# Kernel tuning notes

Hardware: AMD Instinct MI355X
Metric: run time of the kernel (lower is better)

## Reference

```python
import jax, jax.numpy as jnp
import numpy as np

B, Nq, Nk, R = 4, 1024, 1024, 256
NH, DK, DV = 8, 64, 64


def setup_inputs() -> dict:
    key = jax.random.key(0)
    ks = jax.random.split(key, 16)
    mk = lambda k, shape, s=1.0: jax.random.normal(k, shape, dtype=jnp.float32) * s
    inp = {
        'Q_real': mk(ks[0], (B, Nq, R)), 'Q_imag': mk(ks[1], (B, Nq, R)),
        'K_real': mk(ks[2], (B, Nk, R)), 'K_imag': mk(ks[3], (B, Nk, R)),
        'V_real': mk(ks[4], (B, Nk, R)), 'V_imag': mk(ks[5], (B, Nk, R)),
        'WQ_r': mk(ks[6], (NH * DK, R), 0.02), 'WQ_i': mk(ks[7], (NH * DK, R), 0.02),
        'WK_r': mk(ks[8], (NH * DK, R), 0.02), 'WK_i': mk(ks[9], (NH * DK, R), 0.02),
        'WV_r': mk(ks[10], (NH * DV, R), 0.02), 'WV_i': mk(ks[11], (NH * DV, R), 0.02),
        'WO_r': mk(ks[12], (R, NH * DV), 0.02), 'WO_i': mk(ks[13], (R, NH * DV), 0.02),
        'mask': jax.random.randint(ks[14], (B, Nk), 0, 2).astype(bool),
    }
    return inp


def _complex_linear(x, w_r, w_i):
    # x: complex [..., in]; weights real [out, in]. Same math as 4 real matmuls.
    w = (w_r + 1j * w_i).astype(jnp.complex64)
    return x @ w.T


def reference(Q_real, Q_imag, K_real, K_imag, V_real, V_imag,
              WQ_r, WQ_i, WK_r, WK_i, WV_r, WV_i, WO_r, WO_i, mask):
    Q = (Q_real + 1j * Q_imag).astype(jnp.complex64)
    K = (K_real + 1j * K_imag).astype(jnp.complex64)
    V = (V_real + 1j * V_imag).astype(jnp.complex64)

    Qp = _complex_linear(Q, WQ_r, WQ_i).reshape(B, Nq, NH, DK).transpose(0, 2, 1, 3)
    Kp = _complex_linear(K, WK_r, WK_i).reshape(B, Nk, NH, DK).transpose(0, 2, 1, 3)
    Vp = _complex_linear(V, WV_r, WV_i).reshape(B, Nk, NH, DV).transpose(0, 2, 1, 3)

    # complex scores [B, NH, Nq, Nk]; conj on K matches torch .conj().transpose
    scores = jnp.einsum('bhqd,bhkd->bhqk', Qp, jnp.conj(Kp)) / jnp.sqrt(jnp.float32(DK))
    scores_abs = jnp.abs(scores)

    m = mask[:, None, None, :]                    # [B,1,1,Nk]
    valid = jnp.any(mask, axis=-1)[:, None, None, None]  # [B,1,1,1] valid query rows
    masked = jnp.where(m, scores_abs, -jnp.inf)
    # avoid all -inf rows feeding softmax (those rows are zeroed afterwards)
    safe = jnp.where(valid, masked, 0.0)
    w = jax.nn.softmax(safe, axis=-1)
    w = jnp.where(valid, w, 0.0)

    attn = jnp.einsum('bhqk,bhkd->bhqd', w.astype(Vp.dtype), Vp)
    attn = attn.transpose(0, 2, 1, 3).reshape(B, Nq, NH * DV)
    return _complex_linear(attn, WO_r, WO_i)
```

## Files before the change

### kernel.cpp

```cpp
#include <hip/hip_runtime.h>
#include <math.h>

#define NBATCH 4
#define NSEQ   1024
#define RD     256
#define NHEAD  8
#define HD     64
#define NHD    512

typedef __attribute__((ext_vector_type(8))) short  short8;
typedef __attribute__((ext_vector_type(4))) short  short4v;
typedef __attribute__((ext_vector_type(4))) float  float4v;

#define MFMA16(a,b,c) __builtin_amdgcn_mfma_f32_16x16x32_bf16(a,b,c,0,0,0)

typedef const void __attribute__((address_space(1)))* gas_t;
typedef void __attribute__((address_space(3)))* las_t;
#define GLOAD16(g, l) __builtin_amdgcn_global_load_lds((gas_t)(g), (las_t)(l), 16, 0, 0)

static __device__ __forceinline__ unsigned short f2b(float f) {
    union { float f; unsigned u; } x; x.f = f;
    unsigned r = x.u + 0x7fffu + ((x.u >> 16) & 1u);
    return (unsigned short)(r >> 16);
}
static __device__ __forceinline__ void st4(short* dst, float4v v) {
    short4v p;
    p[0] = (short)f2b(v[0]); p[1] = (short)f2b(v[1]);
    p[2] = (short)f2b(v[2]); p[3] = (short)f2b(v[3]);
    *(short4v*)dst = p;
}

struct ConvArgs { const float* src[15]; short* dst[15]; int n4[15]; };

__global__ __launch_bounds__(256) void convert_bf16(ConvArgs ca)
{
    const int a = blockIdx.y;
    if (a == 14) {
        if (blockIdx.x != 0) return;
        __shared__ int isByteLayout;
        const int t = threadIdx.x;
        if (t == 0) isByteLayout = 0;
        __syncthreads();
        const int* mi = (const int*)ca.src[14];
        #pragma unroll
        for (int j = 0; j < 4; j++) {
            int v = mi[t*4 + j];
            if (v & ~1) isByteLayout = 1;
        }
        __syncthreads();
        unsigned char* nm = (unsigned char*)ca.dst[14];
        const unsigned char* mb = (const unsigned char*)ca.src[14];
        if (isByteLayout) {
            #pragma unroll
            for (int j = 0; j < 16; j++) { int k = t*16 + j; nm[k] = mb[k] ? 1 : 0; }
        } else {
            #pragma unroll
            for (int j = 0; j < 16; j++) { int k = t*16 + j; nm[k] = mi[k] ? 1 : 0; }
        }
        return;
    }
    const float* __restrict__ s = ca.src[a];
    short* __restrict__ d = ca.dst[a];
    const int n4 = ca.n4[a];
    for (int i = blockIdx.x*256 + threadIdx.x; i < n4; i += gridDim.x*256) {
        float4v v = *(const float4v*)(s + (size_t)i*4);
        st4(d + (size_t)i*4, v);
    }
}

struct ProjArgs {
    const short* Xr[3]; const short* Xi[3];
    const short* Wr[3]; const short* Wi[3];
    short* Yr[3]; short* Yi[3];
};

__global__ __launch_bounds__(256) void cgemm_proj(ProjArgs pa)
{
    __shared__ short sX[2][128][64];
    __shared__ short sW[2][64][64];
    const int z = blockIdx.z;
    const short* __restrict__ X_r = pa.Xr[z];
    const short* __restrict__ X_i = pa.Xi[z];
    const short* __restrict__ W_r = pa.Wr[z];
    const short* __restrict__ W_i = pa.Wi[z];
    short* __restrict__ Y_r = pa.Yr[z];
    short* __restrict__ Y_i = pa.Yi[z];
    const int transposeOut = (z == 2);

    const int tid  = threadIdx.x;
    const int lane = tid & 63, wave = tid >> 6;
    const int quad = lane >> 4, l16 = lane & 15;
    const int sw8  = l16 & 7;
    const int rsub = lane >> 3;
    const int colg = (lane & 7) ^ rsub;
    const int n0 = blockIdx.x * 64, m0 = blockIdx.y * 128;

    const short nk = (short)0x8000;
    const short8 neg = {nk,nk,nk,nk,nk,nk,nk,nk};

    float4v zf = {0.f,0.f,0.f,0.f};
    float4v Yr[2][4], Yi[2][4];
    #pragma unroll
    for (int ms = 0; ms < 2; ms++)
        #pragma unroll
        for (int t = 0; t < 4; t++) { Yr[ms][t] = zf; Yi[ms][t] = zf; }

    for (int kc = 0; kc < RD; kc += 64) {
        __syncthreads();
        if (wave < 2) {
            const short* gp = wave ? X_i : X_r;
            short* lp = wave ? &sX[1][0][0] : &sX[0][0][0];
            #pragma unroll
            for (int j = 0; j < 16; j++) {
                int row = j*8 + rsub;
                GLOAD16(gp + (size_t)(m0 + row)*RD + kc + colg*8, lp + j*512);
            }
        } else {
            const short* gp = (wave == 3) ? W_i : W_r;
            short* lp = (wave == 3) ? &sW[1][0][0] : &sW[0][0][0];
            #pragma unroll
            for (int j = 0; j < 8; j++) {
                int row = j*8 + rsub;
                GLOAD16(gp + (size_t)(n0 + row)*RD + kc + colg*8, lp + j*512);
            }
        }
        __syncthreads();
        short8 fxr[2][2], fxi[2][2], fxin[2][2];
        #pragma unroll
        for (int ms = 0; ms < 2; ms++)
            #pragma unroll
            for (int ds = 0; ds < 2; ds++) {
                int row = wave*32 + ms*16 + l16;
                int u = ((ds*4 + quad) ^ sw8) * 8;
                fxr[ms][ds]  = *(short8*)&sX[0][row][u];
                fxi[ms][ds]  = *(short8*)&sX[1][row][u];
                fxin[ms][ds] = fxi[ms][ds] ^ neg;
            }
        #pragma unroll
        for (int t = 0; t < 4; t++)
            #pragma unroll
            for (int ds = 0; ds < 2; ds++) {
                int u = ((ds*4 + quad) ^ sw8) * 8;
                short8 wr = *(short8*)&sW[0][t*16 + l16][u];
                short8 wi = *(short8*)&sW[1][t*16 + l16][u];
                #pragma unroll
                for (int ms = 0; ms < 2; ms++) {
                    Yr[ms][t] = MFMA16(fxr[ms][ds],  wr, Yr[ms][t]);
                    Yr[ms][t] = MFMA16(fxin[ms][ds], wi, Yr[ms][t]);
                    Yi[ms][t] = MFMA16(fxr[ms][ds],  wi, Yi[ms][t]);
                    Yi[ms][t] = MFMA16(fxi[ms][ds],  wr, Yi[ms][t]);
                }
            }
    }

    const int b = m0 >> 10, h = n0 >> 6, nb = m0 & 1023;
    short* sT = &sX[0][0][0];
    short* Yp[2] = { Y_r, Y_i };
    #pragma unroll
    for (int p = 0; p < 2; p++) {
        __syncthreads();
        #pragma unroll
        for (int ms = 0; ms < 2; ms++)
            #pragma unroll
            for (int t = 0; t < 4; t++)
                #pragma unroll
                for (int r = 0; r < 4; r++) {
                    float v = p ? Yi[ms][t][r] : Yr[ms][t][r];
                    int rr = wave*32 + ms*16 + quad*4 + r;
                    int cc = t*16 + l16;
                    if (!transposeOut) sT[rr*68 + cc]  = (short)f2b(v);
                    else               sT[cc*132 + rr] = (short)f2b(v);
                }
        __syncthreads();
        #pragma unroll
        for (int it = 0; it < 4; it++) {
            int idx = it*256 + tid;
            int rr, c8;
            size_t o;
            const short* sp;
            if (!transposeOut) {
                rr = idx >> 3; c8 = (idx & 7)*8;
                sp = &sT[rr*68 + c8];
                o = (((size_t)(b*NHEAD + h))*NSEQ + nb + rr)*HD + c8;
            } else {
                rr = idx >> 4; c8 = (idx & 15)*8;
                sp = &sT[rr*132 + c8];
                o = (((size_t)(b*NHEAD + h))*HD + rr)*NSEQ + nb + c8;
            }
            short4v a = *(short4v*)sp;
            short4v bq = *(short4v*)(sp + 4);
            short8 v8 = { a[0],a[1],a[2],a[3], bq[0],bq[1],bq[2],bq[3] };
            *(short8*)&Yp[p][o] = v8;
        }
    }
}

__global__ __launch_bounds__(256) void attn_mfma(
    const short* __restrict__ Qp_r, const short* __restrict__ Qp_i,
    const short* __restrict__ Kp_r, const short* __restrict__ Kp_i,
    const short* __restrict__ Vp_r, const short* __restrict__ Vp_i,
    const unsigned char* __restrict__ mask,
    short* __restrict__ Ar, short* __restrict__ Ai)
{
    __shared__ short sK[2][64][64];
    __shared__ short sV[2][64][64];
    __shared__ short sP[4][16][72];
    __shared__ unsigned char smask[1024];

    const int tid  = threadIdx.x;
    const int lane = tid & 63, wave = tid >> 6;
    const int quad = lane >> 4, l16 = lane & 15;
    const int sw8  = l16 & 7;
    const int qt = blockIdx.x >> 5;
    const int bh = blockIdx.x & 31;
    const int b  = bh >> 3, h = bh & 7;
    const size_t base = (size_t)bh * (NSEQ*HD);

    const int rsub = lane >> 3;
    const int colg = (lane & 7) ^ rsub;

    ((int*)smask)[tid] = ((const int*)(mask + b*NSEQ))[tid];

    {
        const int q0 = qt*64;
        #pragma unroll
        for (int j = 0; j < 4; j++) {
            int c = wave*4 + j;
            const short* gp = (c >> 3) ? Qp_i : Qp_r;
            short* lp = (c >> 3) ? &sK[1][0][0] : &sK[0][0][0];
            int jj = c & 7;
            int row = jj*8 + rsub;
            GLOAD16(gp + base + (size_t)(q0 + row)*HD + colg*8, lp + jj*512);
        }
    }
    __syncthreads();

    short8 fqr[2], fqi[2], fqrn[2];
    {
        const short nk = (short)0x8000;
        short8 neg = {nk,nk,nk,nk,nk,nk,nk,nk};
        const int qrow = wave*16 + l16;
        #pragma unroll
        for (int ds = 0; ds < 2; ds++) {
            int u = ((ds*4 + quad) ^ sw8) * 8;
            fqr[ds]  = *(short8*)&sK[0][qrow][u];
            fqi[ds]  = *(short8*)&sK[1][qrow][u];
            fqrn[ds] = fqr[ds] ^ neg;
        }
    }

    float4v zf = {0.f,0.f,0.f,0.f};
    float4v Or[4], Oi[4];
    float lrow[4];
    #pragma unroll
    for (int t = 0; t < 4; t++) { Or[t] = zf; Oi[t] = zf; }
    #pragma unroll
    for (int r = 0; r < 4; r++) lrow[r] = 0.f;

    const float C2 = 0.18033688f;

    for (int kt = 0; kt < 16; kt++) {
        const int k0 = kt*64;
        __syncthreads();
        {
            const short* gp; short* lp; int isV;
            if      (wave == 0) { gp = Kp_r; lp = &sK[0][0][0]; isV = 0; }
            else if (wave == 1) { gp = Kp_i; lp = &sK[1][0][0]; isV = 0; }
            else if (wave == 2) { gp = Vp_r; lp = &sV[0][0][0]; isV = 1; }
            else                { gp = Vp_i; lp = &sV[1][0][0]; isV = 1; }
            #pragma unroll
            for (int j = 0; j < 8; j++) {
                int row = j*8 + rsub;
                const short* g = isV
                    ? gp + base + (size_t)row*NSEQ + k0 + colg*8
                    : gp + base + (size_t)(k0 + row)*HD + colg*8;
                GLOAD16(g, lp + j*512);
            }
        }
        __syncthreads();

        float4v Sr[4], Si[4];
        #pragma unroll
        for (int t = 0; t < 4; t++) { Sr[t] = zf; Si[t] = zf; }
        #pragma unroll
        for (int t = 0; t < 4; t++)
            #pragma unroll
            for (int ds = 0; ds < 2; ds++) {
                int u = ((ds*4 + quad) ^ sw8) * 8;
                short8 kr = *(short8*)&sK[0][t*16 + l16][u];
                short8 ki = *(short8*)&sK[1][t*16 + l16][u];
                Sr[t] = MFMA16(fqr[ds],  kr, Sr[t]);
                Sr[t] = MFMA16(fqi[ds],  ki, Sr[t]);
                Si[t] = MFMA16(fqi[ds],  kr, Si[t]);
                Si[t] = MFMA16(fqrn[ds], ki, Si[t]);
            }

        #pragma unroll
        for (int t = 0; t < 4; t++) {
            bool mv = smask[k0 + t*16 + l16] != 0;
            #pragma unroll
            for (int r = 0; r < 4; r++) {
                float a = Sr[t][r], c = Si[t][r];
                float x = fmaf(a, a, c*c);
                float s = __builtin_amdgcn_sqrtf(x);
                float e = mv ? __builtin_amdgcn_exp2f(C2 * s) : 0.f;
                lrow[r] += e;
                sP[wave][quad*4 + r][t*16 + l16] = (short)f2b(e);
            }
        }

        #pragma unroll
        for (int ks = 0; ks < 2; ks++) {
            short8 fp = *(short8*)&sP[wave][l16][ks*32 + quad*8];
            #pragma unroll
            for (int t = 0; t < 4; t++) {
                int u = ((ks*4 + quad) ^ sw8) * 8;
                short8 vr = *(short8*)&sV[0][t*16 + l16][u];
                short8 vi = *(short8*)&sV[1][t*16 + l16][u];
                Or[t] = MFMA16(fp, vr, Or[t]);
                Oi[t] = MFMA16(fp, vi, Oi[t]);
            }
        }
    }

    float inv[4];
    #pragma unroll
    for (int r = 0; r < 4; r++) {
        float ls = lrow[r];
        ls += __shfl_xor(ls, 1, 64);
        ls += __shfl_xor(ls, 2, 64);
        ls += __shfl_xor(ls, 4, 64);
        ls += __shfl_xor(ls, 8, 64);
        inv[r] = (ls > 0.f) ? 1.f/ls : 0.f;
    }
    #pragma unroll
    for (int t = 0; t < 4; t++)
        #pragma unroll
        for (int r = 0; r < 4; r++) {
            int q = qt*64 + wave*16 + quad*4 + r;
            int d = t*16 + l16;
            size_t o = ((size_t)(b*NSEQ + q))*NHD + h*HD + d;
            Ar[o] = (short)f2b(Or[t][r] * inv[r]);
            Ai[o] = (short)f2b(Oi[t][r] * inv[r]);
        }
}

__global__ __launch_bounds__(256) void cgemm_out(
    const short* __restrict__ A_r, const short* __restrict__ A_i,
    const short* __restrict__ W_r, const short* __restrict__ W_i,
    float* __restrict__ Out, int writeImagPlane)
{
    __shared__ short sA[2][64][64];
    __shared__ short sW[2][32][64];
    const int tid  = threadIdx.x;
    const int lane = tid & 63, wave = tid >> 6;
    const int quad = lane >> 4, l16 = lane & 15;
    const int sw8  = l16 & 7;
    const int rsub = lane >> 3;
    const int colg = (lane & 7) ^ rsub;
    const int n0 = blockIdx.x * 32, m0 = blockIdx.y * 64;

    const short nk = (short)0x8000;
    const short8 neg = {nk,nk,nk,nk,nk,nk,nk,nk};

    float4v zf = {0.f,0.f,0.f,0.f};
    float4v Yr[2], Yi[2];
    #pragma unroll
    for (int t = 0; t < 2; t++) { Yr[t] = zf; Yi[t] = zf; }

    for (int kc = 0; kc < NHD; kc += 64) {
        __syncthreads();
        {
            if (wave < 2) {
                const short* gp = wave ? A_i : A_r;
                short* lp = wave ? &sA[1][0][0] : &sA[0][0][0];
                #pragma unroll
                for (int j = 0; j < 8; j++) {
                    int row = j*8 + rsub;
                    GLOAD16(gp + (size_t)(m0 + row)*NHD + kc + colg*8, lp + j*512);
                }
            } else {
                const short* gp = (wave == 3) ? W_i : W_r;
                short* lp = (wave == 3) ? &sW[1][0][0] : &sW[0][0][0];
                #pragma unroll
                for (int j = 0; j < 4; j++) {
                    int row = j*8 + rsub;
                    GLOAD16(gp + (size_t)(n0 + row)*NHD + kc + colg*8, lp + j*512);
                }
            }
        }
        __syncthreads();
        short8 far[2], fai[2], fain[2];
        #pragma unroll
        for (int ds = 0; ds < 2; ds++) {
            int u = ((ds*4 + quad) ^ sw8) * 8;
            far[ds]  = *(short8*)&sA[0][wave*16 + l16][u];
            fai[ds]  = *(short8*)&sA[1][wave*16 + l16][u];
            fain[ds] = fai[ds] ^ neg;
        }
        #pragma unroll
        for (int t = 0; t < 2; t++)
            #pragma unroll
            for (int ds = 0; ds < 2; ds++) {
                int u = ((ds*4 + quad) ^ sw8) * 8;
                short8 wr = *(short8*)&sW[0][t*16 + l16][u];
                short8 wi = *(short8*)&sW[1][t*16 + l16][u];
                Yr[t] = MFMA16(far[ds],  wr, Yr[t]);
                Yr[t] = MFMA16(fain[ds], wi, Yr[t]);
                Yi[t] = MFMA16(far[ds],  wi, Yi[t]);
                Yi[t] = MFMA16(fai[ds],  wr, Yi[t]);
            }
    }
    const size_t TOT = (size_t)NBATCH * NSEQ * RD;
    #pragma unroll
    for (int t = 0; t < 2; t++)
        #pragma unroll
        for (int r = 0; r < 4; r++) {
            int row = m0 + wave*16 + quad*4 + r;
            int col = n0 + t*16 + l16;
            size_t o = (size_t)row*RD + col;
            Out[o] = Yr[t][r];
            if (writeImagPlane) Out[o + TOT] = Yi[t][r];
        }
}

extern "C" void kernel_launch(void* const* d_in, const int* in_sizes, int n_in,
                              void* d_out, int out_size, void* d_ws, size_t ws_size,
                              hipStream_t stream)
{
    float* out = (float*)d_out;

    const size_t P = (size_t)NBATCH * NHEAD * NSEQ * HD;
    const size_t H = (size_t)NBATCH * NSEQ * RD;
    const size_t WSZ = (size_t)NHD * RD;

    short* bws = (short*)d_ws;
    short* Qpr = bws + 0*P;  short* Qpi = bws + 1*P;
    short* Kpr = bws + 2*P;  short* Kpi = bws + 3*P;
    short* Vpr = bws + 4*P;  short* Vpi = bws + 5*P;
    short* conv = bws + 6*P;
    short* cX[6]; for (int i = 0; i < 6; i++) cX[i] = conv + i*H;
    short* cW[6]; for (int i = 0; i < 6; i++) cW[i] = conv + 6*H + i*WSZ;
    short* cWOr = conv + 6*H + 6*WSZ;
    short* cWOi = conv + 6*H + 7*WSZ;
    short* Apr = conv;
    short* Api = conv + P;
    unsigned char* nmask = (unsigned char*)(conv + 6*H + 8*WSZ);

    const size_t TOT = (size_t)NBATCH * NSEQ * RD;
    const int writeImagPlane = ((size_t)out_size >= 2*TOT) ? 1 : 0;

    ConvArgs ca;
    for (int i = 0; i < 6; i++) {
        ca.src[i] = (const float*)d_in[i];  ca.dst[i] = cX[i];  ca.n4[i] = (int)(H/4);
    }
    for (int i = 0; i < 6; i++) {
        ca.src[6+i] = (const float*)d_in[6+i]; ca.dst[6+i] = cW[i]; ca.n4[6+i] = (int)(WSZ/4);
    }
    ca.src[12] = (const float*)d_in[12]; ca.dst[12] = cWOr; ca.n4[12] = (int)(WSZ/4);
    ca.src[13] = (const float*)d_in[13]; ca.dst[13] = cWOi; ca.n4[13] = (int)(WSZ/4);
    ca.src[14] = (const float*)d_in[14]; ca.dst[14] = (short*)nmask; ca.n4[14] = 0;

    ProjArgs pa;
    pa.Xr[0] = cX[0]; pa.Xi[0] = cX[1];
    pa.Xr[1] = cX[2]; pa.Xi[1] = cX[3];
    pa.Xr[2] = cX[4]; pa.Xi[2] = cX[5];
    pa.Wr[0] = cW[0]; pa.Wi[0] = cW[1];
    pa.Wr[1] = cW[2]; pa.Wi[1] = cW[3];
    pa.Wr[2] = cW[4]; pa.Wi[2] = cW[5];
    pa.Yr[0] = Qpr; pa.Yi[0] = Qpi;
    pa.Yr[1] = Kpr; pa.Yi[1] = Kpi;
    pa.Yr[2] = Vpr; pa.Yi[2] = Vpi;

    convert_bf16<<<dim3(256, 15), 256, 0, stream>>>(ca);
    cgemm_proj<<<dim3(8, 32, 3), 256, 0, stream>>>(pa);
    attn_mfma<<<dim3(512), 256, 0, stream>>>(Qpr, Qpi, Kpr, Kpi, Vpr, Vpi,
                                             nmask, Apr, Api);
    cgemm_out<<<dim3(8, 64), 256, 0, stream>>>(Apr, Api, cWOr, cWOi, out,
                                               writeImagPlane);
}
```

Measured before the change: 175.4 us.

## Split attention key tiles across wave pairs and merge partial outputs via LDS

The attention kernel now runs 512 threads (8 waves) per block: each query strip of 16 rows is handled by two waves, each taking one half of every 64-key tile. Partial O accumulators and row sums from the second wave are written to shared memory and added by the first wave before normalization and store. This doubles the waves per block to raise latency hiding and MFMA throughput per CU, and spreads tile loads over more waves. In exchange it adds an LDS reduction step, a block-wide sync at the end, and higher register and LDS pressure per block.

```diff
diff --git a/kernel.cpp b/kernel.cpp
--- a/kernel.cpp
+++ b/kernel.cpp
@@ -195,22 +195,25 @@
     }
 }
 
-__global__ __launch_bounds__(256) void attn_mfma(
+__global__ __launch_bounds__(512) void attn_mfma(
     const short* __restrict__ Qp_r, const short* __restrict__ Qp_i,
     const short* __restrict__ Kp_r, const short* __restrict__ Kp_i,
     const short* __restrict__ Vp_r, const short* __restrict__ Vp_i,
     const unsigned char* __restrict__ mask,
     short* __restrict__ Ar, short* __restrict__ Ai)
 {
-    __shared__ short sK[2][64][64];
-    __shared__ short sV[2][64][64];
-    __shared__ short sP[4][16][72];
-    __shared__ unsigned char smask[1024];
+    __shared__ __align__(16) char smem[44032];
+    short (*sK)[64][64] = (short(*)[64][64])smem;
+    short (*sV)[64][64] = (short(*)[64][64])(smem + 16384);
+    short (*sP)[16][40] = (short(*)[16][40])(smem + 32768);
+    unsigned char* smask = (unsigned char*)(smem + 43008);
 
     const int tid  = threadIdx.x;
     const int lane = tid & 63, wave = tid >> 6;
     const int quad = lane >> 4, l16 = lane & 15;
     const int sw8  = l16 & 7;
+    const int qstrip = wave >> 1;
+    const int khalf  = wave & 1;
     const int qt = blockIdx.x >> 5;
     const int bh = blockIdx.x & 31;
     const int b  = bh >> 3, h = bh & 7;
@@ -219,18 +222,17 @@
     const int rsub = lane >> 3;
     const int colg = (lane & 7) ^ rsub;
 
-    ((int*)smask)[tid] = ((const int*)(mask + b*NSEQ))[tid];
+    if (tid < 256) ((int*)smask)[tid] = ((const int*)(mask + b*NSEQ))[tid];
 
     {
         const int q0 = qt*64;
-        #pragma unroll
-        for (int j = 0; j < 4; j++) {
-            int c = wave*4 + j;
-            const short* gp = (c >> 3) ? Qp_i : Qp_r;
-            short* lp = (c >> 3) ? &sK[1][0][0] : &sK[0][0][0];
-            int jj = c & 7;
-            int row = jj*8 + rsub;
-            GLOAD16(gp + base + (size_t)(q0 + row)*HD + colg*8, lp + jj*512);
+        const short* gp = (wave >> 2) ? Qp_i : Qp_r;
+        short* lp = (wave >> 2) ? &sK[1][0][0] : &sK[0][0][0];
+        #pragma unroll
+        for (int jj = 0; jj < 2; jj++) {
+            int j = (wave & 3)*2 + jj;
+            int row = j*8 + rsub;
+            GLOAD16(gp + base + (size_t)(q0 + row)*HD + colg*8, lp + j*512);
         }
     }
     __syncthreads();
@@ -239,7 +241,7 @@
     {
         const short nk = (short)0x8000;
         short8 neg = {nk,nk,nk,nk,nk,nk,nk,nk};
-        const int qrow = wave*16 + l16;
+        const int qrow = qstrip*16 + l16;
         #pragma unroll
         for (int ds = 0; ds < 2; ds++) {
             int u = ((ds*4 + quad) ^ sw8) * 8;
@@ -263,13 +265,15 @@
         const int k0 = kt*64;
         __syncthreads();
         {
+            const int plane = wave >> 1;
             const short* gp; short* lp; int isV;
-            if      (wave == 0) { gp = Kp_r; lp = &sK[0][0][0]; isV = 0; }
-            else if (wave == 1) { gp = Kp_i; lp = &sK[1][0][0]; isV = 0; }
-            else if (wave == 2) { gp = Vp_r; lp = &sV[0][0][0]; isV = 1; }
-            else                { gp = Vp_i; lp = &sV[1][0][0]; isV = 1; }
-            #pragma unroll
-            for (int j = 0; j < 8; j++) {
+            if      (plane == 0) { gp = Kp_r; lp = &sK[0][0][0]; isV = 0; }
+            else if (plane == 1) { gp = Kp_i; lp = &sK[1][0][0]; isV = 0; }
+            else if (plane == 2) { gp = Vp_r; lp = &sV[0][0][0]; isV = 1; }
+            else                 { gp = Vp_i; lp = &sV[1][0][0]; isV = 1; }
+            #pragma unroll
+            for (int jj = 0; jj < 4; jj++) {
+                int j = (wave & 1)*4 + jj;
                 int row = j*8 + rsub;
                 const short* g = isV
                     ? gp + base + (size_t)row*NSEQ + k0 + colg*8
@@ -279,16 +283,16 @@
         }
         __syncthreads();
 
-        float4v Sr[4], Si[4];
-        #pragma unroll
-        for (int t = 0; t < 4; t++) { Sr[t] = zf; Si[t] = zf; }
-        #pragma unroll
-        for (int t = 0; t < 4; t++)
+        float4v Sr[2], Si[2];
+        Sr[0] = zf; Sr[1] = zf; Si[0] = zf; Si[1] = zf;
+        #pragma unroll
+        for (int t = 0; t < 2; t++)
             #pragma unroll
             for (int ds = 0; ds < 2; ds++) {
                 int u = ((ds*4 + quad) ^ sw8) * 8;
-                short8 kr = *(short8*)&sK[0][t*16 + l16][u];
-                short8 ki = *(short8*)&sK[1][t*16 + l16][u];
+                int krow = khalf*32 + t*16 + l16;
+                short8 kr = *(short8*)&sK[0][krow][u];
+                short8 ki = *(short8*)&sK[1][krow][u];
                 Sr[t] = MFMA16(fqr[ds],  kr, Sr[t]);
                 Sr[t] = MFMA16(fqi[ds],  ki, Sr[t]);
                 Si[t] = MFMA16(fqi[ds],  kr, Si[t]);
@@ -296,8 +300,8 @@
             }
 
         #pragma unroll
-        for (int t = 0; t < 4; t++) {
-            bool mv = smask[k0 + t*16 + l16] != 0;
+        for (int t = 0; t < 2; t++) {
+            bool mv = smask[k0 + khalf*32 + t*16 + l16] != 0;
             #pragma unroll
             for (int r = 0; r < 4; r++) {
                 float a = Sr[t][r], c = Si[t][r];
@@ -309,12 +313,11 @@
             }
         }
 
-        #pragma unroll
-        for (int ks = 0; ks < 2; ks++) {
-            short8 fp = *(short8*)&sP[wave][l16][ks*32 + quad*8];
+        {
+            short8 fp = *(short8*)&sP[wave][l16][quad*8];
             #pragma unroll
             for (int t = 0; t < 4; t++) {
-                int u = ((ks*4 + quad) ^ sw8) * 8;
+                int u = ((khalf*4 + quad) ^ sw8) * 8;
                 short8 vr = *(short8*)&sV[0][t*16 + l16][u];
                 short8 vi = *(short8*)&sV[1][t*16 + l16][u];
                 Or[t] = MFMA16(fp, vr, Or[t]);
@@ -323,26 +326,54 @@
         }
     }
 
-    float inv[4];
-    #pragma unroll
-    for (int r = 0; r < 4; r++) {
-        float ls = lrow[r];
-        ls += __shfl_xor(ls, 1, 64);
-        ls += __shfl_xor(ls, 2, 64);
-        ls += __shfl_xor(ls, 4, 64);
-        ls += __shfl_xor(ls, 8, 64);
-        inv[r] = (ls > 0.f) ? 1.f/ls : 0.f;
-    }
-    #pragma unroll
-    for (int t = 0; t < 4; t++)
+    __syncthreads();
+    float* sC = (float*)smem;
+    float* sL = (float*)(smem + 32768);
+    if (khalf == 1) {
+        #pragma unroll
+        for (int t = 0; t < 4; t++)
+            #pragma unroll
+            for (int r = 0; r < 4; r++) {
+                int o8 = ((qstrip*4 + t)*64 + lane)*8 + r*2;
+                sC[o8]     = Or[t][r];
+                sC[o8 + 1] = Oi[t][r];
+            }
+        int lo = (qstrip*64 + lane)*4;
+        #pragma unroll
+        for (int r = 0; r < 4; r++) sL[lo + r] = lrow[r];
+    }
+    __syncthreads();
+    if (khalf == 0) {
+        #pragma unroll
+        for (int t = 0; t < 4; t++)
+            #pragma unroll
+            for (int r = 0; r < 4; r++) {
+                int o8 = ((qstrip*4 + t)*64 + lane)*8 + r*2;
+                Or[t][r] += sC[o8];
+                Oi[t][r] += sC[o8 + 1];
+            }
+        int lo = (qstrip*64 + lane)*4;
+        float inv[4];
         #pragma unroll
         for (int r = 0; r < 4; r++) {
-            int q = qt*64 + wave*16 + quad*4 + r;
-            int d = t*16 + l16;
-            size_t o = ((size_t)(b*NSEQ + q))*NHD + h*HD + d;
-            Ar[o] = (short)f2b(Or[t][r] * inv[r]);
-            Ai[o] = (short)f2b(Oi[t][r] * inv[r]);
-        }
+            float ls = lrow[r] + sL[lo + r];
+            ls += __shfl_xor(ls, 1, 64);
+            ls += __shfl_xor(ls, 2, 64);
+            ls += __shfl_xor(ls, 4, 64);
+            ls += __shfl_xor(ls, 8, 64);
+            inv[r] = (ls > 0.f) ? 1.f/ls : 0.f;
+        }
+        #pragma unroll
+        for (int t = 0; t < 4; t++)
+            #pragma unroll
+            for (int r = 0; r < 4; r++) {
+                int q = qt*64 + qstrip*16 + quad*4 + r;
+                int d = t*16 + l16;
+                size_t o = ((size_t)(b*NSEQ + q))*NHD + h*HD + d;
+                Ar[o] = (short)f2b(Or[t][r] * inv[r]);
+                Ai[o] = (short)f2b(Oi[t][r] * inv[r]);
+            }
+    }
 }
 
 __global__ __launch_bounds__(256) void cgemm_out(
@@ -474,7 +505,7 @@
 
     convert_bf16<<<dim3(256, 15), 256, 0, stream>>>(ca);
     cgemm_proj<<<dim3(8, 32, 3), 256, 0, stream>>>(pa);
-    attn_mfma<<<dim3(512), 256, 0, stream>>>(Qpr, Qpi, Kpr, Kpi, Vpr, Vpi,
+    attn_mfma<<<dim3(512), 512, 0, stream>>>(Qpr, Qpi, Kpr, Kpi, Vpr, Vpi,
                                              nmask, Apr, Api);
     cgemm_out<<<dim3(8, 64), 256, 0, stream>>>(Apr, Api, cWOr, cWOi, out,
                                                writeImagPlane);
```

Result: no change. 174.1 us (-0.7%).

## Switch attention kernel to 32x32x16 MFMA with split-key waves and LDS reduction

Applied to the files above, without the earlier changes.

The attention kernel now uses 32x32x16 bf16 MFMA instead of 16x16x32. Each wave handles a 32-query by 32-key quadrant, so waves are split by query half and key half. Q fragments are loaded directly from global memory rather than staged through LDS. Partial outputs and row sums from the two key-half waves are combined through shared memory at the end. The aim is fewer MFMA instructions and LDS fragment reads per tile, at the cost of more registers, a final cross-wave reduction, and a larger shared-memory footprint.

```diff
diff --git a/kernel.cpp b/kernel.cpp
--- a/kernel.cpp
+++ b/kernel.cpp
@@ -8,11 +8,13 @@
 #define HD     64
 #define NHD    512
 
-typedef __attribute__((ext_vector_type(8))) short  short8;
-typedef __attribute__((ext_vector_type(4))) short  short4v;
-typedef __attribute__((ext_vector_type(4))) float  float4v;
+typedef __attribute__((ext_vector_type(8)))  short  short8;
+typedef __attribute__((ext_vector_type(4)))  short  short4v;
+typedef __attribute__((ext_vector_type(4)))  float  float4v;
+typedef __attribute__((ext_vector_type(16))) float  float16v;
 
 #define MFMA16(a,b,c) __builtin_amdgcn_mfma_f32_16x16x32_bf16(a,b,c,0,0,0)
+#define MFMA32(a,b,c) __builtin_amdgcn_mfma_f32_32x32x16_bf16(a,b,c,0,0,0)
 
 typedef const void __attribute__((address_space(1)))* gas_t;
 typedef void __attribute__((address_space(3)))* las_t;
@@ -202,15 +204,19 @@
     const unsigned char* __restrict__ mask,
     short* __restrict__ Ar, short* __restrict__ Ai)
 {
-    __shared__ short sK[2][64][64];
-    __shared__ short sV[2][64][64];
-    __shared__ short sP[4][16][72];
-    __shared__ unsigned char smask[1024];
+    __shared__ __align__(16) char smem[44032];
+    short (*sK)[64][64] = (short(*)[64][64])smem;
+    short (*sV)[64][64] = (short(*)[64][64])(smem + 16384);
+    short (*sP)[32][40] = (short(*)[32][40])(smem + 32768);
+    unsigned char* smask = (unsigned char*)(smem + 43008);
 
     const int tid  = threadIdx.x;
     const int lane = tid & 63, wave = tid >> 6;
-    const int quad = lane >> 4, l16 = lane & 15;
-    const int sw8  = l16 & 7;
+    const int l32  = lane & 31;
+    const int lh   = lane >> 5;
+    const int sw7  = lane & 7;
+    const int qhalf = wave >> 1;
+    const int khalf = wave & 1;
     const int qt = blockIdx.x >> 5;
     const int bh = blockIdx.x & 31;
     const int b  = bh >> 3, h = bh & 7;
@@ -221,41 +227,26 @@
 
     ((int*)smask)[tid] = ((const int*)(mask + b*NSEQ))[tid];
 
-    {
-        const int q0 = qt*64;
-        #pragma unroll
-        for (int j = 0; j < 4; j++) {
-            int c = wave*4 + j;
-            const short* gp = (c >> 3) ? Qp_i : Qp_r;
-            short* lp = (c >> 3) ? &sK[1][0][0] : &sK[0][0][0];
-            int jj = c & 7;
-            int row = jj*8 + rsub;
-            GLOAD16(gp + base + (size_t)(q0 + row)*HD + colg*8, lp + jj*512);
-        }
-    }
-    __syncthreads();
-
-    short8 fqr[2], fqi[2], fqrn[2];
-    {
-        const short nk = (short)0x8000;
-        short8 neg = {nk,nk,nk,nk,nk,nk,nk,nk};
-        const int qrow = wave*16 + l16;
-        #pragma unroll
-        for (int ds = 0; ds < 2; ds++) {
-            int u = ((ds*4 + quad) ^ sw8) * 8;
-            fqr[ds]  = *(short8*)&sK[0][qrow][u];
-            fqi[ds]  = *(short8*)&sK[1][qrow][u];
-            fqrn[ds] = fqr[ds] ^ neg;
-        }
-    }
-
-    float4v zf = {0.f,0.f,0.f,0.f};
-    float4v Or[4], Oi[4];
-    float lrow[4];
-    #pragma unroll
-    for (int t = 0; t < 4; t++) { Or[t] = zf; Oi[t] = zf; }
-    #pragma unroll
-    for (int r = 0; r < 4; r++) lrow[r] = 0.f;
+    const short* sgp = (wave == 0) ? Kp_r : (wave == 1) ? Kp_i
+                     : (wave == 2) ? Vp_r : Vp_i;
+    const int sisV = (wave >= 2);
+    short* slp = (short*)(smem + wave*8192);
+
+    const short nk = (short)0x8000;
+    const short8 neg = {nk,nk,nk,nk,nk,nk,nk,nk};
+    short8 fqr[4], fqi[4], fqrn[4];
+    #pragma unroll
+    for (int c = 0; c < 4; c++) {
+        size_t qo = base + (size_t)(qt*64 + qhalf*32 + l32)*HD + c*16 + lh*8;
+        fqr[c]  = *(const short8*)&Qp_r[qo];
+        fqi[c]  = *(const short8*)&Qp_i[qo];
+        fqrn[c] = fqr[c] ^ neg;
+    }
+
+    float16v Or0 = {0}, Or1 = {0}, Oi0 = {0}, Oi1 = {0};
+    float lrow[16];
+    #pragma unroll
+    for (int r = 0; r < 16; r++) lrow[r] = 0.f;
 
     const float C2 = 0.18033688f;
 
@@ -263,86 +254,99 @@
         const int k0 = kt*64;
         __syncthreads();
         {
-            const short* gp; short* lp; int isV;
-            if      (wave == 0) { gp = Kp_r; lp = &sK[0][0][0]; isV = 0; }
-            else if (wave == 1) { gp = Kp_i; lp = &sK[1][0][0]; isV = 0; }
-            else if (wave == 2) { gp = Vp_r; lp = &sV[0][0][0]; isV = 1; }
-            else                { gp = Vp_i; lp = &sV[1][0][0]; isV = 1; }
             #pragma unroll
             for (int j = 0; j < 8; j++) {
                 int row = j*8 + rsub;
-                const short* g = isV
-                    ? gp + base + (size_t)row*NSEQ + k0 + colg*8
-                    : gp + base + (size_t)(k0 + row)*HD + colg*8;
-                GLOAD16(g, lp + j*512);
-            }
-        }
-        __syncthreads();
-
-        float4v Sr[4], Si[4];
-        #pragma unroll
-        for (int t = 0; t < 4; t++) { Sr[t] = zf; Si[t] = zf; }
-        #pragma unroll
-        for (int t = 0; t < 4; t++)
-            #pragma unroll
-            for (int ds = 0; ds < 2; ds++) {
-                int u = ((ds*4 + quad) ^ sw8) * 8;
-                short8 kr = *(short8*)&sK[0][t*16 + l16][u];
-                short8 ki = *(short8*)&sK[1][t*16 + l16][u];
-                Sr[t] = MFMA16(fqr[ds],  kr, Sr[t]);
-                Sr[t] = MFMA16(fqi[ds],  ki, Sr[t]);
-                Si[t] = MFMA16(fqi[ds],  kr, Si[t]);
-                Si[t] = MFMA16(fqrn[ds], ki, Si[t]);
-            }
-
-        #pragma unroll
-        for (int t = 0; t < 4; t++) {
-            bool mv = smask[k0 + t*16 + l16] != 0;
-            #pragma unroll
-            for (int r = 0; r < 4; r++) {
-                float a = Sr[t][r], c = Si[t][r];
-                float x = fmaf(a, a, c*c);
-                float s = __builtin_amdgcn_sqrtf(x);
-                float e = mv ? __builtin_amdgcn_exp2f(C2 * s) : 0.f;
-                lrow[r] += e;
-                sP[wave][quad*4 + r][t*16 + l16] = (short)f2b(e);
-            }
-        }
-
-        #pragma unroll
-        for (int ks = 0; ks < 2; ks++) {
-            short8 fp = *(short8*)&sP[wave][l16][ks*32 + quad*8];
-            #pragma unroll
-            for (int t = 0; t < 4; t++) {
-                int u = ((ks*4 + quad) ^ sw8) * 8;
-                short8 vr = *(short8*)&sV[0][t*16 + l16][u];
-                short8 vi = *(short8*)&sV[1][t*16 + l16][u];
-                Or[t] = MFMA16(fp, vr, Or[t]);
-                Oi[t] = MFMA16(fp, vi, Oi[t]);
-            }
-        }
-    }
-
-    float inv[4];
-    #pragma unroll
-    for (int r = 0; r < 4; r++) {
-        float ls = lrow[r];
-        ls += __shfl_xor(ls, 1, 64);
-        ls += __shfl_xor(ls, 2, 64);
-        ls += __shfl_xor(ls, 4, 64);
-        ls += __shfl_xor(ls, 8, 64);
-        inv[r] = (ls > 0.f) ? 1.f/ls : 0.f;
-    }
-    #pragma unroll
-    for (int t = 0; t < 4; t++)
-        #pragma unroll
-        for (int r = 0; r < 4; r++) {
-            int q = qt*64 + wave*16 + quad*4 + r;
-            int d = t*16 + l16;
-            size_t o = ((size_t)(b*NSEQ + q))*NHD + h*HD + d;
-            Ar[o] = (short)f2b(Or[t][r] * inv[r]);
-            Ai[o] = (short)f2b(Oi[t][r] * inv[r]);
-        }
+                const short* g = sisV
+                    ? sgp + base + (size_t)row*NSEQ + k0 + colg*8
+                    : sgp + base + (size_t)(k0 + row)*HD + colg*8;
+                GLOAD16(g, slp + j*512);
+            }
+        }
+        __syncthreads();
+
+        float16v Sr = {0}, Si = {0};
+        const int krow = khalf*32 + l32;
+        #pragma unroll
+        for (int c = 0; c < 4; c++) {
+            int u = ((c*2 + lh) ^ sw7) * 8;
+            short8 kr = *(short8*)&sK[0][krow][u];
+            short8 ki = *(short8*)&sK[1][krow][u];
+            Sr = MFMA32(fqr[c],  kr, Sr);
+            Sr = MFMA32(fqi[c],  ki, Sr);
+            Si = MFMA32(fqi[c],  kr, Si);
+            Si = MFMA32(fqrn[c], ki, Si);
+        }
+
+        bool mv = smask[k0 + khalf*32 + l32] != 0;
+        #pragma unroll
+        for (int r = 0; r < 16; r++) {
+            float a = Sr[r], c = Si[r];
+            float x = fmaf(a, a, c*c);
+            float s = __builtin_amdgcn_sqrtf(x);
+            float e = mv ? __builtin_amdgcn_exp2f(C2 * s) : 0.f;
+            lrow[r] += e;
+            int row = (r & 3) + 8*(r >> 2) + 4*lh;
+            sP[wave][row][l32] = (short)f2b(e);
+        }
+
+        #pragma unroll
+        for (int c = 0; c < 2; c++) {
+            short8 fp = *(short8*)&sP[wave][l32][c*16 + lh*8];
+            #pragma unroll
+            for (int dt = 0; dt < 2; dt++) {
+                int vrow = dt*32 + l32;
+                int u = ((khalf*4 + c*2 + lh) ^ sw7) * 8;
+                short8 vr = *(short8*)&sV[0][vrow][u];
+                short8 vi = *(short8*)&sV[1][vrow][u];
+                if (dt == 0) { Or0 = MFMA32(fp, vr, Or0); Oi0 = MFMA32(fp, vi, Oi0); }
+                else         { Or1 = MFMA32(fp, vr, Or1); Oi1 = MFMA32(fp, vi, Oi1); }
+            }
+        }
+    }
+
+    __syncthreads();
+    float* sC = (float*)smem;
+    float* sL = (float*)(smem + 32768);
+    if (khalf == 1) {
+        #pragma unroll
+        for (int r = 0; r < 16; r++) {
+            int o0 = (qhalf*2048 + r*64 + lane)*2;
+            sC[o0]          = Or0[r];
+            sC[o0 + 1]      = Oi0[r];
+            int o1 = (qhalf*2048 + 1024 + r*64 + lane)*2;
+            sC[o1]          = Or1[r];
+            sC[o1 + 1]      = Oi1[r];
+            sL[(qhalf*16 + r)*64 + lane] = lrow[r];
+        }
+    }
+    __syncthreads();
+    if (khalf == 0) {
+        float inv[16];
+        #pragma unroll
+        for (int r = 0; r < 16; r++) {
+            int o0 = (qhalf*2048 + r*64 + lane)*2;
+            Or0[r] += sC[o0];     Oi0[r] += sC[o0 + 1];
+            int o1 = (qhalf*2048 + 1024 + r*64 + lane)*2;
+            Or1[r] += sC[o1];     Oi1[r] += sC[o1 + 1];
+            float ls = lrow[r] + sL[(qhalf*16 + r)*64 + lane];
+            ls += __shfl_xor(ls, 1,  64);
+            ls += __shfl_xor(ls, 2,  64);
+            ls += __shfl_xor(ls, 4,  64);
+            ls += __shfl_xor(ls, 8,  64);
+            ls += __shfl_xor(ls, 16, 64);
+            inv[r] = (ls > 0.f) ? 1.f/ls : 0.f;
+        }
+        #pragma unroll
+        for (int r = 0; r < 16; r++) {
+            int q = qt*64 + qhalf*32 + (r & 3) + 8*(r >> 2) + 4*lh;
+            size_t o = ((size_t)(b*NSEQ + q))*NHD + h*HD;
+            Ar[o + l32]      = (short)f2b(Or0[r] * inv[r]);
+            Ai[o + l32]      = (short)f2b(Oi0[r] * inv[r]);
+            Ar[o + 32 + l32] = (short)f2b(Or1[r] * inv[r]);
+            Ai[o + 32 + l32] = (short)f2b(Oi1[r] * inv[r]);
+        }
+    }
 }
 
 __global__ __launch_bounds__(256) void cgemm_out(
```

New measurement: 176.8 us. No clear change (+0.8%).
